# Performance work log

Hardware: AMD Instinct MI355X
Metric: run time of the kernel (lower is better)

Reference implementation:

```python
import jax, jax.numpy as jnp
import numpy as np

NUM_USERS = 50000
NUM_ITEMS = 50000
EMBED_DIM = 128
NUM_LAYERS = 3
NUM_EDGES = 600000
N_NODES = NUM_USERS + NUM_ITEMS


def setup_inputs() -> dict:
    key = jax.random.key(0)
    k1, k2, k3, k4, k5 = jax.random.split(key, 5)
    edge_index = jax.random.randint(k1, (2, NUM_EDGES), 0, N_NODES, dtype=jnp.int64 if jax.config.x64_enabled else jnp.int32)
    user_emb = jax.random.normal(k2, (NUM_USERS, EMBED_DIM), jnp.float32) * 0.1
    item_emb = jax.random.normal(k3, (NUM_ITEMS, EMBED_DIM), jnp.float32) * 0.1
    Wa = jax.random.normal(k4, (NUM_LAYERS, 2 * EMBED_DIM, 1), jnp.float32) * 0.05
    ba = jnp.zeros((NUM_LAYERS, 1), jnp.float32)
    Wg = jax.random.normal(k5, (NUM_LAYERS, 2 * EMBED_DIM, EMBED_DIM), jnp.float32) * 0.05
    bg = jnp.zeros((NUM_LAYERS, EMBED_DIM), jnp.float32)
    return {"edge_index": edge_index, "user_emb": user_emb, "item_emb": item_emb,
            "Wa": Wa, "ba": ba, "Wg": Wg, "bg": bg}


def reference(edge_index, user_emb, item_emb, Wa, ba, Wg, bg):
    U = user_emb.shape[0]
    N = U + item_emb.shape[0]
    src, dst = edge_index[0], edge_index[1]
    x = jnp.concatenate([user_emb, item_emb], axis=0)  # [N, d]
    for l in range(Wa.shape[0]):
        src_emb = x[src]                                # [E, d] gather
        dst_emb = x[dst]                                # [E, d] gather
        cat = jnp.concatenate([src_emb, dst_emb], 1)    # [E, 2d]
        att = jax.nn.sigmoid(cat @ Wa[l] + ba[l])       # [E, 1]
        # attention-weighted scatter-sum over destination node (zeros for isolated nodes)
        agg = jax.ops.segment_sum(src_emb * att, dst, num_segments=N)  # [N, d]
        x = jax.nn.relu(jnp.concatenate([x, agg], 1) @ Wg[l] + bg[l])  # [N, d]
    return x[:U], x[U:]
```

## Files before the change

### kernel.cpp

```cpp
#include <hip/hip_runtime.h>
#include <cstddef>
#include <cstdint>

#define NUSERS 50000
#define NITEMS 50000
#define NNODES 100000
#define DIM    128
#define NLAYERS 3
#define NEDGES 600000
#define NPAD 100096

#define EBLK  8192
#define NBLK  74
#define NBUCK 782

typedef __attribute__((ext_vector_type(8))) short short8;
typedef __attribute__((ext_vector_type(4))) float f32x4;

__device__ __forceinline__ float bf_lo(unsigned u) { return __uint_as_float(u << 16); }
__device__ __forceinline__ float bf_hi(unsigned u) { return __uint_as_float(u & 0xffff0000u); }
__device__ __forceinline__ unsigned short f2bf(float f) {
    unsigned b = __float_as_uint(f);
    return (unsigned short)((b + 0x7fffu + ((b >> 16) & 1u)) >> 16);
}

__device__ __forceinline__ void async16(const void* g, void* l) {
    __builtin_amdgcn_global_load_lds(
        (const __attribute__((address_space(1))) unsigned int*)(uintptr_t)g,
        (__attribute__((address_space(3))) unsigned int*)(unsigned int)(uintptr_t)l,
        16, 0, 0);
}

__global__ __launch_bounds__(256) void concat_dots_kernel(
        const float* __restrict__ ue, const float* __restrict__ ie,
        const float* __restrict__ Wa, const float* __restrict__ ba,
        unsigned short* __restrict__ xb,
        float* __restrict__ a_src, float* __restrict__ a_dst) {
    const int n = blockIdx.x * 16 + (threadIdx.x >> 4);
    if (n >= NNODES) return;
    const int sub = threadIdx.x & 15;
    const float* r = (n < NUSERS) ? (ue + (size_t)n * DIM)
                                  : (ie + (size_t)(n - NUSERS) * DIM);
    const float4 v0 = *(const float4*)(r + sub * 8);
    const float4 v1 = *(const float4*)(r + sub * 8 + 4);
    const float4 wl0 = *(const float4*)(Wa + sub * 8);
    const float4 wl1 = *(const float4*)(Wa + sub * 8 + 4);
    const float4 wh0 = *(const float4*)(Wa + DIM + sub * 8);
    const float4 wh1 = *(const float4*)(Wa + DIM + sub * 8 + 4);

    uint4 o;
    o.x = ((unsigned)f2bf(v0.y) << 16) | (unsigned)f2bf(v0.x);
    o.y = ((unsigned)f2bf(v0.w) << 16) | (unsigned)f2bf(v0.z);
    o.z = ((unsigned)f2bf(v1.y) << 16) | (unsigned)f2bf(v1.x);
    o.w = ((unsigned)f2bf(v1.w) << 16) | (unsigned)f2bf(v1.z);
    *(uint4*)(xb + (size_t)n * DIM + sub * 8) = o;

    float ps = v0.x * wl0.x + v0.y * wl0.y + v0.z * wl0.z + v0.w * wl0.w
             + v1.x * wl1.x + v1.y * wl1.y + v1.z * wl1.z + v1.w * wl1.w;
    float pd = v0.x * wh0.x + v0.y * wh0.y + v0.z * wh0.z + v0.w * wh0.w
             + v1.x * wh1.x + v1.y * wh1.y + v1.z * wh1.z + v1.w * wh1.w;
    #pragma unroll
    for (int off = 1; off < 16; off <<= 1) {
        ps += __shfl_xor(ps, off);
        pd += __shfl_xor(pd, off);
    }
    if (sub == 0) { a_src[n] = ps; a_dst[n] = pd + ba[0]; }
}

__global__ void wg_conv_kernel(const float* __restrict__ Wg,
                               unsigned short* __restrict__ Bf) {
    const int tid = blockIdx.x * blockDim.x + threadIdx.x;
    if (tid >= NLAYERS * 4096) return;
    const int l    = tid >> 12;
    const int slot = tid & 4095;
    const int lane = slot & 63;
    const int t2   = slot >> 6;
    const int nf   = t2 & 3;
    const int t3   = t2 >> 2;
    const int ks   = t3 & 7;
    const int nb   = t3 >> 3;
    const int col  = nb * 64 + nf * 16 + (lane & 15);
    const int k0   = ks * 32 + (lane >> 4) * 8;
    const float* wsrc = Wg + (size_t)l * 256 * DIM;
    unsigned short o[8];
    #pragma unroll
    for (int j = 0; j < 8; ++j) o[j] = f2bf(wsrc[(size_t)(k0 + j) * DIM + col]);
    *(short8*)(Bf + (size_t)tid * 8) = *(short8*)o;
}

__global__ __launch_bounds__(256) void bin_count_kernel(
        const int* __restrict__ dst, unsigned* __restrict__ counts) {
    __shared__ unsigned hist[NBUCK];
    for (int i = threadIdx.x; i < NBUCK; i += 256) hist[i] = 0;
    __syncthreads();
    const int base = blockIdx.x * EBLK;
    const int end  = (base + EBLK < NEDGES) ? base + EBLK : NEDGES;
    for (int e = base + threadIdx.x; e < end; e += 256)
        atomicAdd(&hist[dst[e] >> 7], 1u);
    __syncthreads();
    for (int i = threadIdx.x; i < NBUCK; i += 256)
        counts[(size_t)blockIdx.x * NBUCK + i] = hist[i];
}

__global__ __launch_bounds__(1024) void prefix_kernel(
        unsigned* __restrict__ counts, unsigned* __restrict__ bucketbase) {
    const int b = threadIdx.x;
    unsigned tot = 0;
    if (b < NBUCK) {
        for (int i = 0; i < NBLK; ++i) {
            const unsigned c = counts[(size_t)i * NBUCK + b];
            counts[(size_t)i * NBUCK + b] = tot;
            tot += c;
        }
    }
    const int lane = b & 63, w = b >> 6;
    unsigned s = tot;
    #pragma unroll
    for (int o = 1; o < 64; o <<= 1) {
        unsigned t = (unsigned)__shfl_up((int)s, o);
        if (lane >= o) s += t;
    }
    __shared__ unsigned wsum[16];
    if (lane == 63) wsum[w] = s;
    __syncthreads();
    unsigned add = 0;
    #pragma unroll
    for (int j = 0; j < 15; ++j) if (w > j) add += wsum[j];
    if (b < NBUCK) bucketbase[b] = s + add - tot;
    if (b == NBUCK - 1) bucketbase[NBUCK] = s + add;
}

__global__ __launch_bounds__(256) void bin_scatter_kernel(
        const int* __restrict__ src, const int* __restrict__ dst,
        const unsigned* __restrict__ counts, const unsigned* __restrict__ bucketbase,
        unsigned* __restrict__ pairs) {
    __shared__ unsigned off[NBUCK];
    for (int i = threadIdx.x; i < NBUCK; i += 256)
        off[i] = bucketbase[i] + counts[(size_t)blockIdx.x * NBUCK + i];
    __syncthreads();
    const int base = blockIdx.x * EBLK;
    const int end  = (base + EBLK < NEDGES) ? base + EBLK : NEDGES;
    for (int e = base + threadIdx.x; e < end; e += 256) {
        const int d = dst[e];
        const unsigned pos = atomicAdd(&off[d >> 7], 1u);
        pairs[pos] = ((unsigned)(d & 127) << 17) | (unsigned)src[e];
    }
}

__global__ __launch_bounds__(256) void bucket_csr_kernel(
        const unsigned* __restrict__ pairs, const unsigned* __restrict__ bucketbase,
        int* __restrict__ row_start, int* __restrict__ csr_src) {
    __shared__ unsigned deg[128], rs[128], fill[128];
    const int b = blockIdx.x;
    const unsigned seg0 = bucketbase[b], seg1 = bucketbase[b + 1];
    const int t = threadIdx.x;
    if (t < 128) deg[t] = 0;
    __syncthreads();
    for (unsigned i = seg0 + t; i < seg1; i += 256)
        atomicAdd(&deg[pairs[i] >> 17], 1u);
    __syncthreads();
    if (t < 128) rs[t] = deg[t];
    __syncthreads();
    #pragma unroll
    for (int o = 1; o < 128; o <<= 1) {
        unsigned tmp = 0;
        if (t < 128 && t >= o) tmp = rs[t - o];
        __syncthreads();
        if (t < 128) rs[t] += tmp;
        __syncthreads();
    }
    if (t < 128) {
        const unsigned excl = rs[t] - deg[t];
        fill[t] = excl;
        const int node = b * 128 + t;
        if (node < NNODES) row_start[node] = (int)(seg0 + excl);
    }
    __syncthreads();
    for (unsigned i = seg0 + t; i < seg1; i += 256) {
        const unsigned p = pairs[i];
        const unsigned r = atomicAdd(&fill[p >> 17], 1u);
        csr_src[seg0 + r] = (int)(p & 0x1ffffu);
    }
    if (b == 0 && t == 0) row_start[NNODES] = NEDGES;
}

__global__ __launch_bounds__(256) void pull_agg_kernel(
        const int* __restrict__ row_start, const int* __restrict__ csr_src,
        const float* __restrict__ a_src, const float* __restrict__ a_dst,
        const unsigned short* __restrict__ xb, unsigned short* __restrict__ aggb) {
    const int n = blockIdx.x * 16 + (threadIdx.x >> 4);
    if (n >= NNODES) return;
    const int lane = threadIdx.x & 63;
    const int sub  = lane & 15;
    const int qb   = lane & 48;
    const int beg = row_start[n], end = row_start[n + 1];
    const float adst = a_dst[n];

    float a0 = 0, a1 = 0, a2 = 0, a3 = 0, a4 = 0, a5 = 0, a6 = 0, a7 = 0;

    for (int base = beg; base < end; base += 16) {
        const int rem = end - base;
        const int cnt = rem < 16 ? rem : 16;
        int   idx_l = 0;
        float att_l = 0.0f;
        if (sub < cnt) {
            idx_l = csr_src[base + sub];
            att_l = 1.0f / (1.0f + __expf(-(a_src[idx_l] + adst)));
        }
        int i = 0;
        for (; i + 3 < cnt; i += 4) {
            const int   s0 = __shfl(idx_l, qb + i);
            const int   s1 = __shfl(idx_l, qb + i + 1);
            const int   s2 = __shfl(idx_l, qb + i + 2);
            const int   s3 = __shfl(idx_l, qb + i + 3);
            const float w0 = __shfl(att_l, qb + i);
            const float w1 = __shfl(att_l, qb + i + 1);
            const float w2 = __shfl(att_l, qb + i + 2);
            const float w3 = __shfl(att_l, qb + i + 3);
            const uint4 u0 = *(const uint4*)(xb + (size_t)s0 * DIM + sub * 8);
            const uint4 u1 = *(const uint4*)(xb + (size_t)s1 * DIM + sub * 8);
            const uint4 u2 = *(const uint4*)(xb + (size_t)s2 * DIM + sub * 8);
            const uint4 u3 = *(const uint4*)(xb + (size_t)s3 * DIM + sub * 8);
            a0 += bf_lo(u0.x) * w0 + bf_lo(u1.x) * w1 + bf_lo(u2.x) * w2 + bf_lo(u3.x) * w3;
            a1 += bf_hi(u0.x) * w0 + bf_hi(u1.x) * w1 + bf_hi(u2.x) * w2 + bf_hi(u3.x) * w3;
            a2 += bf_lo(u0.y) * w0 + bf_lo(u1.y) * w1 + bf_lo(u2.y) * w2 + bf_lo(u3.y) * w3;
            a3 += bf_hi(u0.y) * w0 + bf_hi(u1.y) * w1 + bf_hi(u2.y) * w2 + bf_hi(u3.y) * w3;
            a4 += bf_lo(u0.z) * w0 + bf_lo(u1.z) * w1 + bf_lo(u2.z) * w2 + bf_lo(u3.z) * w3;
            a5 += bf_hi(u0.z) * w0 + bf_hi(u1.z) * w1 + bf_hi(u2.z) * w2 + bf_hi(u3.z) * w3;
            a6 += bf_lo(u0.w) * w0 + bf_lo(u1.w) * w1 + bf_lo(u2.w) * w2 + bf_lo(u3.w) * w3;
            a7 += bf_hi(u0.w) * w0 + bf_hi(u1.w) * w1 + bf_hi(u2.w) * w2 + bf_hi(u3.w) * w3;
        }
        for (; i < cnt; ++i) {
            const int   s = __shfl(idx_l, qb + i);
            const float w = __shfl(att_l, qb + i);
            const uint4 u = *(const uint4*)(xb + (size_t)s * DIM + sub * 8);
            a0 += bf_lo(u.x) * w;  a1 += bf_hi(u.x) * w;
            a2 += bf_lo(u.y) * w;  a3 += bf_hi(u.y) * w;
            a4 += bf_lo(u.z) * w;  a5 += bf_hi(u.z) * w;
            a6 += bf_lo(u.w) * w;  a7 += bf_hi(u.w) * w;
        }
    }

    uint4 o;
    o.x = ((unsigned)f2bf(a1) << 16) | (unsigned)f2bf(a0);
    o.y = ((unsigned)f2bf(a3) << 16) | (unsigned)f2bf(a2);
    o.z = ((unsigned)f2bf(a5) << 16) | (unsigned)f2bf(a4);
    o.w = ((unsigned)f2bf(a7) << 16) | (unsigned)f2bf(a6);
    *(uint4*)(aggb + (size_t)n * DIM + sub * 8) = o;
}

__global__ __launch_bounds__(256, 4) void gemm_mfma_kernel(
        unsigned short* __restrict__ xb, const unsigned short* __restrict__ aggb,
        const unsigned short* __restrict__ bfr, const float* __restrict__ bg,
        const float* __restrict__ wa_next, const float* __restrict__ ba_next,
        float* __restrict__ a_src, float* __restrict__ a_dst,
        float* __restrict__ xout_f32, int write_f32, int do_dots) {
    __shared__ unsigned short At[2][64 * 128];
    __shared__ float psS[2][64], psD[2][64];

    const int tid  = threadIdx.x;
    const int lane = tid & 63;
    const int wid  = tid >> 6;
    const int mbase = blockIdx.x * 64;

    #pragma unroll
    for (int h = 0; h < 2; ++h) {
        const unsigned short* s = h ? aggb : xb;
        #pragma unroll
        for (int i = 0; i < 4; ++i) {
            const int lrow = i * 16 + wid * 4 + (lane >> 4);
            const int c    = (lane & 15) ^ (lrow & 7);
            async16(s + (size_t)(mbase + lrow) * DIM + c * 8,
                    &At[h][(i * 16 + wid * 4) * 128]);
        }
    }

    const int waveM = wid >> 1, waveN = wid & 1;
    const int l16 = lane & 15, kq = lane >> 4;
    const unsigned short* bfw = bfr + (size_t)(waveN * 8) * 4 * 64 * 8;

    f32x4 acc[2][4] = {};
    short8 bcur[4], bnxt[4];

    asm volatile("s_waitcnt vmcnt(4)" ::: "memory");
    __builtin_amdgcn_s_barrier();

    #pragma unroll
    for (int nf = 0; nf < 4; ++nf)
        bcur[nf] = *(const short8*)(bfw + ((size_t)(0 * 4 + nf) * 64 + lane) * 8);

    #pragma unroll
    for (int ks = 0; ks < 8; ++ks) {
        if (ks == 4) {
            asm volatile("s_waitcnt vmcnt(0)" ::: "memory");
            __builtin_amdgcn_s_barrier();
        }
        if (ks < 7) {
            #pragma unroll
            for (int nf = 0; nf < 4; ++nf)
                bnxt[nf] = *(const short8*)(bfw + ((size_t)((ks + 1) * 4 + nf) * 64 + lane) * 8);
        }
        const int h = ks >> 2, ksl = ks & 3;
        short8 a[2];
        #pragma unroll
        for (int mf = 0; mf < 2; ++mf) {
            const int row   = waveM * 32 + mf * 16 + l16;
            const int chunk = (ksl * 4 + kq) ^ (row & 7);
            a[mf] = *(const short8*)&At[h][row * 128 + chunk * 8];
        }
        #pragma unroll
        for (int mf = 0; mf < 2; ++mf)
            #pragma unroll
            for (int nf = 0; nf < 4; ++nf)
                acc[mf][nf] = __builtin_amdgcn_mfma_f32_16x16x32_bf16(
                    a[mf], bcur[nf], acc[mf][nf], 0, 0, 0);
        if (ks < 7) {
            #pragma unroll
            for (int nf = 0; nf < 4; ++nf) bcur[nf] = bnxt[nf];
        }
    }

    const int rsub = kq * 4;
    float waS[4] = {0, 0, 0, 0}, waD[4] = {0, 0, 0, 0}, bias[4];
    #pragma unroll
    for (int nf = 0; nf < 4; ++nf) {
        const int col = waveN * 64 + nf * 16 + l16;
        bias[nf] = bg[col];
        if (do_dots) { waS[nf] = wa_next[col]; waD[nf] = wa_next[DIM + col]; }
    }
    #pragma unroll
    for (int mf = 0; mf < 2; ++mf) {
        #pragma unroll
        for (int j = 0; j < 4; ++j) {
            const int row = mbase + waveM * 32 + mf * 16 + rsub + j;
            float s = 0.0f, d = 0.0f;
            #pragma unroll
            for (int nf = 0; nf < 4; ++nf) {
                const int col = waveN * 64 + nf * 16 + l16;
                const float v = fmaxf(acc[mf][nf][j] + bias[nf], 0.0f);
                if (write_f32) {
                    if (row < NNODES) xout_f32[(size_t)row * DIM + col] = v;
                } else {
                    const unsigned short bv = f2bf(v);
                    const unsigned pb = (unsigned)(unsigned short)__shfl_xor((int)bv, 1);
                    if (!(l16 & 1) && row < NNODES)
                        *(unsigned*)(xb + (size_t)row * DIM + col) =
                            (unsigned)bv | (pb << 16);
                }
                s += v * waS[nf];
                d += v * waD[nf];
            }
            if (do_dots) {
                #pragma unroll
                for (int off = 1; off < 16; off <<= 1) {
                    s += __shfl_xor(s, off);
                    d += __shfl_xor(d, off);
                }
                if (l16 == 0) {
                    const int rl = waveM * 32 + mf * 16 + rsub + j;
                    psS[waveN][rl] = s;
                    psD[waveN][rl] = d;
                }
            }
        }
    }
    if (do_dots) {
        __syncthreads();
        if (tid < 64) {
            const int row = mbase + tid;
            if (row < NNODES) {
                a_src[row] = psS[0][tid] + psS[1][tid];
                a_dst[row] = psD[0][tid] + psD[1][tid] + ba_next[0];
            }
        }
    }
}

extern "C" void kernel_launch(void* const* d_in, const int* in_sizes, int n_in,
                              void* d_out, int out_size, void* d_ws, size_t ws_size,
                              hipStream_t stream) {
    const int*   edge = (const int*)d_in[0];
    const float* ue   = (const float*)d_in[1];
    const float* ie   = (const float*)d_in[2];
    const float* Wa   = (const float*)d_in[3];
    const float* ba   = (const float*)d_in[4];
    const float* Wg   = (const float*)d_in[5];
    const float* bg   = (const float*)d_in[6];

    const int* src = edge;
    const int* dst = edge + NEDGES;

    float* x = (float*)d_out;

    unsigned short* xb   = (unsigned short*)d_ws;
    unsigned short* aggb = xb + (size_t)NPAD * DIM;
    unsigned short* bfr  = aggb + (size_t)NPAD * DIM;
    float* a_src      = (float*)(bfr + NLAYERS * 32768);
    float* a_dst      = a_src + NPAD;
    int*   row_start  = (int*)(a_dst + NPAD);
    int*   csr_src    = row_start + NPAD + 256;
    unsigned* pairs   = (unsigned*)(csr_src + NEDGES);
    unsigned* counts  = pairs + NEDGES;
    unsigned* bbase   = counts + (size_t)NBLK * NBUCK;

    concat_dots_kernel<<<(NNODES + 15) / 16, 256, 0, stream>>>(
        ue, ie, Wa, ba, xb, a_src, a_dst);
    wg_conv_kernel<<<(NLAYERS * 4096 + 255) / 256, 256, 0, stream>>>(Wg, bfr);

    bin_count_kernel<<<NBLK, 256, 0, stream>>>(dst, counts);
    prefix_kernel<<<1, 1024, 0, stream>>>(counts, bbase);
    bin_scatter_kernel<<<NBLK, 256, 0, stream>>>(src, dst, counts, bbase, pairs);
    bucket_csr_kernel<<<NBUCK, 256, 0, stream>>>(pairs, bbase, row_start, csr_src);

    const int gemm_blocks = (NNODES + 63) / 64;
    const int pull_blocks = (NNODES + 15) / 16;
    for (int l = 0; l < NLAYERS; ++l) {
        pull_agg_kernel<<<pull_blocks, 256, 0, stream>>>(
            row_start, csr_src, a_src, a_dst, xb, aggb);
        const int last = (l == NLAYERS - 1);
        gemm_mfma_kernel<<<gemm_blocks, 256, 0, stream>>>(
            xb, aggb, bfr + (size_t)l * 32768, bg + (size_t)l * DIM,
            Wa + (size_t)(l + 1 < NLAYERS ? l + 1 : 0) * 256,
            ba + (l + 1 < NLAYERS ? l + 1 : 0),
            a_src, a_dst, x, last ? 1 : 0, last ? 0 : 1);
    }
}
```

Before: 230.7 us.

## Merge prologue kernels into one launch and shrink GEMM tile to 32 rows

The concat/dot, weight conversion and bin-count kernels become one prologue kernel that dispatches on block index, saving two launches. The GEMM tile drops from 64 to 32 rows, with four waves each covering 32 output columns. B fragments are now loaded per k-step with no register double-buffering, and launch bounds rise to 7 blocks per SM to raise occupancy. Row bounds checks are removed because the node count divides evenly by 32; the cost is more blocks and more repeated B loads per row.

```diff
diff --git a/kernel.cpp b/kernel.cpp
--- a/kernel.cpp
+++ b/kernel.cpp
@@ -14,6 +14,10 @@
 #define NBLK  74
 #define NBUCK 782
 
+#define PRO_CONCAT 6250
+#define PRO_WG     48
+#define PRO_TOTAL  (PRO_CONCAT + PRO_WG + NBLK)
+
 typedef __attribute__((ext_vector_type(8))) short short8;
 typedef __attribute__((ext_vector_type(4))) float f32x4;
 
@@ -31,75 +35,76 @@
         16, 0, 0);
 }
 
-__global__ __launch_bounds__(256) void concat_dots_kernel(
+__global__ __launch_bounds__(256) void prologue_kernel(
         const float* __restrict__ ue, const float* __restrict__ ie,
         const float* __restrict__ Wa, const float* __restrict__ ba,
+        const float* __restrict__ Wg, const int* __restrict__ dst,
         unsigned short* __restrict__ xb,
-        float* __restrict__ a_src, float* __restrict__ a_dst) {
-    const int n = blockIdx.x * 16 + (threadIdx.x >> 4);
-    if (n >= NNODES) return;
-    const int sub = threadIdx.x & 15;
-    const float* r = (n < NUSERS) ? (ue + (size_t)n * DIM)
-                                  : (ie + (size_t)(n - NUSERS) * DIM);
-    const float4 v0 = *(const float4*)(r + sub * 8);
-    const float4 v1 = *(const float4*)(r + sub * 8 + 4);
-    const float4 wl0 = *(const float4*)(Wa + sub * 8);
-    const float4 wl1 = *(const float4*)(Wa + sub * 8 + 4);
-    const float4 wh0 = *(const float4*)(Wa + DIM + sub * 8);
-    const float4 wh1 = *(const float4*)(Wa + DIM + sub * 8 + 4);
-
-    uint4 o;
-    o.x = ((unsigned)f2bf(v0.y) << 16) | (unsigned)f2bf(v0.x);
-    o.y = ((unsigned)f2bf(v0.w) << 16) | (unsigned)f2bf(v0.z);
-    o.z = ((unsigned)f2bf(v1.y) << 16) | (unsigned)f2bf(v1.x);
-    o.w = ((unsigned)f2bf(v1.w) << 16) | (unsigned)f2bf(v1.z);
-    *(uint4*)(xb + (size_t)n * DIM + sub * 8) = o;
-
-    float ps = v0.x * wl0.x + v0.y * wl0.y + v0.z * wl0.z + v0.w * wl0.w
-             + v1.x * wl1.x + v1.y * wl1.y + v1.z * wl1.z + v1.w * wl1.w;
-    float pd = v0.x * wh0.x + v0.y * wh0.y + v0.z * wh0.z + v0.w * wh0.w
-             + v1.x * wh1.x + v1.y * wh1.y + v1.z * wh1.z + v1.w * wh1.w;
-    #pragma unroll
-    for (int off = 1; off < 16; off <<= 1) {
-        ps += __shfl_xor(ps, off);
-        pd += __shfl_xor(pd, off);
-    }
-    if (sub == 0) { a_src[n] = ps; a_dst[n] = pd + ba[0]; }
-}
-
-__global__ void wg_conv_kernel(const float* __restrict__ Wg,
-                               unsigned short* __restrict__ Bf) {
-    const int tid = blockIdx.x * blockDim.x + threadIdx.x;
-    if (tid >= NLAYERS * 4096) return;
-    const int l    = tid >> 12;
-    const int slot = tid & 4095;
-    const int lane = slot & 63;
-    const int t2   = slot >> 6;
-    const int nf   = t2 & 3;
-    const int t3   = t2 >> 2;
-    const int ks   = t3 & 7;
-    const int nb   = t3 >> 3;
-    const int col  = nb * 64 + nf * 16 + (lane & 15);
-    const int k0   = ks * 32 + (lane >> 4) * 8;
-    const float* wsrc = Wg + (size_t)l * 256 * DIM;
-    unsigned short o[8];
-    #pragma unroll
-    for (int j = 0; j < 8; ++j) o[j] = f2bf(wsrc[(size_t)(k0 + j) * DIM + col]);
-    *(short8*)(Bf + (size_t)tid * 8) = *(short8*)o;
-}
-
-__global__ __launch_bounds__(256) void bin_count_kernel(
-        const int* __restrict__ dst, unsigned* __restrict__ counts) {
+        float* __restrict__ a_src, float* __restrict__ a_dst,
+        unsigned short* __restrict__ Bf, unsigned* __restrict__ counts) {
     __shared__ unsigned hist[NBUCK];
-    for (int i = threadIdx.x; i < NBUCK; i += 256) hist[i] = 0;
-    __syncthreads();
-    const int base = blockIdx.x * EBLK;
-    const int end  = (base + EBLK < NEDGES) ? base + EBLK : NEDGES;
-    for (int e = base + threadIdx.x; e < end; e += 256)
-        atomicAdd(&hist[dst[e] >> 7], 1u);
-    __syncthreads();
-    for (int i = threadIdx.x; i < NBUCK; i += 256)
-        counts[(size_t)blockIdx.x * NBUCK + i] = hist[i];
+    const int blk = blockIdx.x;
+
+    if (blk < PRO_CONCAT) {
+        const int n = blk * 16 + (threadIdx.x >> 4);
+        if (n >= NNODES) return;
+        const int sub = threadIdx.x & 15;
+        const float* r = (n < NUSERS) ? (ue + (size_t)n * DIM)
+                                      : (ie + (size_t)(n - NUSERS) * DIM);
+        const float4 v0 = *(const float4*)(r + sub * 8);
+        const float4 v1 = *(const float4*)(r + sub * 8 + 4);
+        const float4 wl0 = *(const float4*)(Wa + sub * 8);
+        const float4 wl1 = *(const float4*)(Wa + sub * 8 + 4);
+        const float4 wh0 = *(const float4*)(Wa + DIM + sub * 8);
+        const float4 wh1 = *(const float4*)(Wa + DIM + sub * 8 + 4);
+
+        uint4 o;
+        o.x = ((unsigned)f2bf(v0.y) << 16) | (unsigned)f2bf(v0.x);
+        o.y = ((unsigned)f2bf(v0.w) << 16) | (unsigned)f2bf(v0.z);
+        o.z = ((unsigned)f2bf(v1.y) << 16) | (unsigned)f2bf(v1.x);
+        o.w = ((unsigned)f2bf(v1.w) << 16) | (unsigned)f2bf(v1.z);
+        *(uint4*)(xb + (size_t)n * DIM + sub * 8) = o;
+
+        float ps = v0.x * wl0.x + v0.y * wl0.y + v0.z * wl0.z + v0.w * wl0.w
+                 + v1.x * wl1.x + v1.y * wl1.y + v1.z * wl1.z + v1.w * wl1.w;
+        float pd = v0.x * wh0.x + v0.y * wh0.y + v0.z * wh0.z + v0.w * wh0.w
+                 + v1.x * wh1.x + v1.y * wh1.y + v1.z * wh1.z + v1.w * wh1.w;
+        #pragma unroll
+        for (int off = 1; off < 16; off <<= 1) {
+            ps += __shfl_xor(ps, off);
+            pd += __shfl_xor(pd, off);
+        }
+        if (sub == 0) { a_src[n] = ps; a_dst[n] = pd + ba[0]; }
+    } else if (blk < PRO_CONCAT + PRO_WG) {
+        const int tid = (blk - PRO_CONCAT) * 256 + threadIdx.x;
+        if (tid >= NLAYERS * 4096) return;
+        const int l    = tid >> 12;
+        const int slot = tid & 4095;
+        const int lane = slot & 63;
+        const int t2   = slot >> 6;
+        const int nf   = t2 & 3;
+        const int t3   = t2 >> 2;
+        const int ks   = t3 & 7;
+        const int nb   = t3 >> 3;
+        const int col  = nb * 64 + nf * 16 + (lane & 15);
+        const int k0   = ks * 32 + (lane >> 4) * 8;
+        const float* wsrc = Wg + (size_t)l * 256 * DIM;
+        unsigned short o[8];
+        #pragma unroll
+        for (int j = 0; j < 8; ++j) o[j] = f2bf(wsrc[(size_t)(k0 + j) * DIM + col]);
+        *(short8*)(Bf + (size_t)tid * 8) = *(short8*)o;
+    } else {
+        const int bblk = blk - PRO_CONCAT - PRO_WG;
+        for (int i = threadIdx.x; i < NBUCK; i += 256) hist[i] = 0;
+        __syncthreads();
+        const int base = bblk * EBLK;
+        const int end  = (base + EBLK < NEDGES) ? base + EBLK : NEDGES;
+        for (int e = base + threadIdx.x; e < end; e += 256)
+            atomicAdd(&hist[dst[e] >> 7], 1u);
+        __syncthreads();
+        for (int i = threadIdx.x; i < NBUCK; i += 256)
+            counts[(size_t)bblk * NBUCK + i] = hist[i];
+    }
 }
 
 __global__ __launch_bounds__(1024) void prefix_kernel(
@@ -249,25 +254,25 @@
     *(uint4*)(aggb + (size_t)n * DIM + sub * 8) = o;
 }
 
-__global__ __launch_bounds__(256, 4) void gemm_mfma_kernel(
+__global__ __launch_bounds__(256, 7) void gemm_mfma_kernel(
         unsigned short* __restrict__ xb, const unsigned short* __restrict__ aggb,
         const unsigned short* __restrict__ bfr, const float* __restrict__ bg,
         const float* __restrict__ wa_next, const float* __restrict__ ba_next,
         float* __restrict__ a_src, float* __restrict__ a_dst,
         float* __restrict__ xout_f32, int write_f32, int do_dots) {
-    __shared__ unsigned short At[2][64 * 128];
-    __shared__ float psS[2][64], psD[2][64];
+    __shared__ unsigned short At[2][32 * 128];
+    __shared__ float psS[4][32], psD[4][32];
 
     const int tid  = threadIdx.x;
     const int lane = tid & 63;
     const int wid  = tid >> 6;
-    const int mbase = blockIdx.x * 64;
+    const int mbase = blockIdx.x * 32;
 
     #pragma unroll
     for (int h = 0; h < 2; ++h) {
         const unsigned short* s = h ? aggb : xb;
         #pragma unroll
-        for (int i = 0; i < 4; ++i) {
+        for (int i = 0; i < 2; ++i) {
             const int lrow = i * 16 + wid * 4 + (lane >> 4);
             const int c    = (lane & 15) ^ (lrow & 7);
             async16(s + (size_t)(mbase + lrow) * DIM + c * 8,
@@ -275,19 +280,14 @@
         }
     }
 
-    const int waveM = wid >> 1, waveN = wid & 1;
     const int l16 = lane & 15, kq = lane >> 4;
-    const unsigned short* bfw = bfr + (size_t)(waveN * 8) * 4 * 64 * 8;
-
-    f32x4 acc[2][4] = {};
-    short8 bcur[4], bnxt[4];
-
-    asm volatile("s_waitcnt vmcnt(4)" ::: "memory");
+    const unsigned short* bfw = bfr + (size_t)(wid >> 1) * (8 * 4 * 64 * 8);
+    const int nfo = (wid & 1) * 2;
+
+    f32x4 acc[2][2] = {};
+
+    asm volatile("s_waitcnt vmcnt(2)" ::: "memory");
     __builtin_amdgcn_s_barrier();
-
-    #pragma unroll
-    for (int nf = 0; nf < 4; ++nf)
-        bcur[nf] = *(const short8*)(bfw + ((size_t)(0 * 4 + nf) * 64 + lane) * 8);
 
     #pragma unroll
     for (int ks = 0; ks < 8; ++ks) {
@@ -295,36 +295,30 @@
             asm volatile("s_waitcnt vmcnt(0)" ::: "memory");
             __builtin_amdgcn_s_barrier();
         }
-        if (ks < 7) {
-            #pragma unroll
-            for (int nf = 0; nf < 4; ++nf)
-                bnxt[nf] = *(const short8*)(bfw + ((size_t)((ks + 1) * 4 + nf) * 64 + lane) * 8);
-        }
         const int h = ks >> 2, ksl = ks & 3;
-        short8 a[2];
+        short8 b[2], a[2];
+        #pragma unroll
+        for (int nf = 0; nf < 2; ++nf)
+            b[nf] = *(const short8*)(bfw + ((size_t)(ks * 4 + nfo + nf) * 64 + lane) * 8);
         #pragma unroll
         for (int mf = 0; mf < 2; ++mf) {
-            const int row   = waveM * 32 + mf * 16 + l16;
+            const int row   = mf * 16 + l16;
             const int chunk = (ksl * 4 + kq) ^ (row & 7);
             a[mf] = *(const short8*)&At[h][row * 128 + chunk * 8];
         }
         #pragma unroll
         for (int mf = 0; mf < 2; ++mf)
             #pragma unroll
-            for (int nf = 0; nf < 4; ++nf)
+            for (int nf = 0; nf < 2; ++nf)
                 acc[mf][nf] = __builtin_amdgcn_mfma_f32_16x16x32_bf16(
-                    a[mf], bcur[nf], acc[mf][nf], 0, 0, 0);
-        if (ks < 7) {
-            #pragma unroll
-            for (int nf = 0; nf < 4; ++nf) bcur[nf] = bnxt[nf];
-        }
+                    a[mf], b[nf], acc[mf][nf], 0, 0, 0);
     }
 
     const int rsub = kq * 4;
-    float waS[4] = {0, 0, 0, 0}, waD[4] = {0, 0, 0, 0}, bias[4];
-    #pragma unroll
-    for (int nf = 0; nf < 4; ++nf) {
-        const int col = waveN * 64 + nf * 16 + l16;
+    float waS[2] = {0, 0}, waD[2] = {0, 0}, bias[2];
+    #pragma unroll
+    for (int nf = 0; nf < 2; ++nf) {
+        const int col = wid * 32 + nf * 16 + l16;
         bias[nf] = bg[col];
         if (do_dots) { waS[nf] = wa_next[col]; waD[nf] = wa_next[DIM + col]; }
     }
@@ -332,18 +326,18 @@
     for (int mf = 0; mf < 2; ++mf) {
         #pragma unroll
         for (int j = 0; j < 4; ++j) {
-            const int row = mbase + waveM * 32 + mf * 16 + rsub + j;
+            const int row = mbase + mf * 16 + rsub + j;
             float s = 0.0f, d = 0.0f;
             #pragma unroll
-            for (int nf = 0; nf < 4; ++nf) {
-                const int col = waveN * 64 + nf * 16 + l16;
+            for (int nf = 0; nf < 2; ++nf) {
+                const int col = wid * 32 + nf * 16 + l16;
                 const float v = fmaxf(acc[mf][nf][j] + bias[nf], 0.0f);
                 if (write_f32) {
-                    if (row < NNODES) xout_f32[(size_t)row * DIM + col] = v;
+                    xout_f32[(size_t)row * DIM + col] = v;
                 } else {
                     const unsigned short bv = f2bf(v);
                     const unsigned pb = (unsigned)(unsigned short)__shfl_xor((int)bv, 1);
-                    if (!(l16 & 1) && row < NNODES)
+                    if (!(l16 & 1))
                         *(unsigned*)(xb + (size_t)row * DIM + col) =
                             (unsigned)bv | (pb << 16);
                 }
@@ -357,21 +351,20 @@
                     d += __shfl_xor(d, off);
                 }
                 if (l16 == 0) {
-                    const int rl = waveM * 32 + mf * 16 + rsub + j;
-                    psS[waveN][rl] = s;
-                    psD[waveN][rl] = d;
+                    const int rl = mf * 16 + rsub + j;
+                    psS[wid][rl] = s;
+                    psD[wid][rl] = d;
                 }
             }
         }
     }
     if (do_dots) {
         __syncthreads();
-        if (tid < 64) {
+        if (tid < 32) {
             const int row = mbase + tid;
-            if (row < NNODES) {
-                a_src[row] = psS[0][tid] + psS[1][tid];
-                a_dst[row] = psD[0][tid] + psD[1][tid] + ba_next[0];
-            }
+            a_src[row] = psS[0][tid] + psS[1][tid] + psS[2][tid] + psS[3][tid];
+            a_dst[row] = psD[0][tid] + psD[1][tid] + psD[2][tid] + psD[3][tid]
+                       + ba_next[0];
         }
     }
 }
@@ -403,16 +396,14 @@
     unsigned* counts  = pairs + NEDGES;
     unsigned* bbase   = counts + (size_t)NBLK * NBUCK;
 
-    concat_dots_kernel<<<(NNODES + 15) / 16, 256, 0, stream>>>(
-        ue, ie, Wa, ba, xb, a_src, a_dst);
-    wg_conv_kernel<<<(NLAYERS * 4096 + 255) / 256, 256, 0, stream>>>(Wg, bfr);
-
-    bin_count_kernel<<<NBLK, 256, 0, stream>>>(dst, counts);
+    prologue_kernel<<<PRO_TOTAL, 256, 0, stream>>>(
+        ue, ie, Wa, ba, Wg, dst, xb, a_src, a_dst, bfr, counts);
+
     prefix_kernel<<<1, 1024, 0, stream>>>(counts, bbase);
     bin_scatter_kernel<<<NBLK, 256, 0, stream>>>(src, dst, counts, bbase, pairs);
     bucket_csr_kernel<<<NBUCK, 256, 0, stream>>>(pairs, bbase, row_start, csr_src);
 
-    const int gemm_blocks = (NNODES + 63) / 64;
+    const int gemm_blocks = NNODES / 32;
     const int pull_blocks = (NNODES + 15) / 16;
     for (int l = 0; l < NLAYERS; ++l) {
         pull_agg_kernel<<<pull_blocks, 256, 0, stream>>>(
```

Measured after the change: 222.8 us. 3.4% less time.
